# Kernel tuning notes

Measured on AMD Instinct MI355X. Metric: run time of the kernel, lower is better.

## Reference

```python
import jax, jax.numpy as jnp
import numpy as np

E = 2048      # embedding_size
H = 16        # num_heads
D = 128       # head_dim
G = 4         # gqa_factor
KH = H // G   # kv heads
F = 8192      # up_proj_size
B, S = 2, 2048


def _layer_norm(x, g, b, eps=1e-5):
    mu = jnp.mean(x, axis=-1, keepdims=True)
    var = jnp.mean(jnp.square(x - mu), axis=-1, keepdims=True)
    return (x - mu) * jax.lax.rsqrt(var + eps) * g + b


def setup_inputs() -> dict:
    key = jax.random.key(0)
    ks = jax.random.split(key, 16)
    std = 0.02
    inp = {
        'x': jax.random.normal(ks[0], (B, S, E), dtype=jnp.float32),
        'ln1_g': jnp.ones((E,), jnp.float32),
        'ln1_b': jnp.zeros((E,), jnp.float32),
        'wq': jax.random.normal(ks[1], (E, H * D), jnp.float32) * std,
        'bq': jnp.zeros((H * D,), jnp.float32),
        'wk': jax.random.normal(ks[2], (E, KH * D), jnp.float32) * std,
        'bk': jnp.zeros((KH * D,), jnp.float32),
        'wv': jax.random.normal(ks[3], (E, KH * D), jnp.float32) * std,
        'bv': jnp.zeros((KH * D,), jnp.float32),
        'wo': jax.random.normal(ks[4], (H * D, E), jnp.float32) * std,
        'bo': jnp.zeros((E,), jnp.float32),
        'ln2_g': jnp.ones((E,), jnp.float32),
        'ln2_b': jnp.zeros((E,), jnp.float32),
        'wu': jax.random.normal(ks[5], (E, F), jnp.float32) * std,
        'bu': jnp.zeros((F,), jnp.float32),
        'wd': jax.random.normal(ks[6], (F, E), jnp.float32) * std,
        'bd': jnp.zeros((E,), jnp.float32),
    }
    return inp


def _block(x, ln1_g, ln1_b, wq, bq, wk, bk, wv, bv, wo, bo, ln2_g, ln2_b, wu, bu, wd, bd):
    b, s, e = x.shape
    # attention sub-block (use_cache=False, train_mode=False -> no dropout)
    x1 = _layer_norm(x, ln1_g, ln1_b)
    q = (x1 @ wq + bq).reshape(b, s, H, D).transpose(0, 2, 1, 3)       # (B,H,S,D)
    q = q.reshape(b, KH, G, s, D)                                       # (B,KH,G,S,D)
    k = (x1 @ wk + bk).reshape(b, s, KH, D).transpose(0, 2, 1, 3)      # (B,KH,S,D)
    v = (x1 @ wv + bv).reshape(b, s, KH, D).transpose(0, 2, 1, 3)      # (B,KH,S,D)
    scores = jnp.einsum('bkgsd,bktd->bkgst', q, k) / np.sqrt(D).astype(np.float32)
    causal = jnp.tril(jnp.ones((s, s), dtype=bool))                     # True = keep
    scores = jnp.where(causal, scores, -jnp.inf)
    att = jax.nn.softmax(scores, axis=-1)
    o = jnp.einsum('bkgst,bktd->bkgsd', att, v)                         # (B,KH,G,S,D)
    o = o.reshape(b, H, s, D).transpose(0, 2, 1, 3).reshape(b, s, H * D)
    x = x + (o @ wo + bo)
    # MLP sub-block
    x2 = _layer_norm(x, ln2_g, ln2_b)
    h = jax.nn.gelu(x2 @ wu + bu, approximate=False)
    x = x + (h @ wd + bd)
    return x


def reference(x, ln1_g, ln1_b, wq, bq, wk, bk, wv, bv, wo, bo, ln2_g, ln2_b, wu, bu, wd, bd):
    return _block(x, ln1_g, ln1_b, wq, bq, wk, bk, wv, bv, wo, bo, ln2_g, ln2_b, wu, bu, wd, bd)
```

## Files before the change

kernel.cpp:

```cpp
#include <hip/hip_runtime.h>
#include <hip/hip_bf16.h>
#include <cstdint>
#include <math.h>

typedef unsigned short u16;
using f32x4   = __attribute__((ext_vector_type(4))) float;
using short8  = __attribute__((ext_vector_type(8))) short;
using short4v = __attribute__((ext_vector_type(4))) short;

#define DEV static __device__ __forceinline__

DEV u16 f2bf(float f) {
  union { float f; unsigned u; } v; v.f = f;
  unsigned r = v.u + 0x7fffu + ((v.u >> 16) & 1u);
  return (u16)(r >> 16);
}

DEV f32x4 mfma_bf16(short8 a, short8 b, f32x4 c) {
  return __builtin_amdgcn_mfma_f32_16x16x32_bf16(a, b, c, 0, 0, 0);
}

DEV void gload16(const void* g, void* l) {
  __builtin_amdgcn_global_load_lds((const __attribute__((address_space(1))) void*)g,
                                   (__attribute__((address_space(3))) void*)l,
                                   16, 0, 0);
}

__global__ __launch_bounds__(256) void prep_kernel(
    const float* __restrict__ x, const float* __restrict__ g,
    const float* __restrict__ bt, u16* __restrict__ x1,
    const float* __restrict__ wq, const float* __restrict__ wk,
    const float* __restrict__ wv, const float* __restrict__ wo,
    const float* __restrict__ wu, const float* __restrict__ wd,
    u16* __restrict__ wqT, u16* __restrict__ wkT, u16* __restrict__ wvT,
    u16* __restrict__ woT, u16* __restrict__ wuT, u16* __restrict__ wdT)
{
  __shared__ float sm[32 * 33];
  int bid = blockIdx.x;
  const int t = threadIdx.x;

  if (bid < 4096) {
    const int lane = t & 63, w = t >> 6;
    const float* xr = x + (size_t)bid * 2048 + t * 8;
    float v[8];
    {
      const float4* p4 = (const float4*)xr;
      float4 a = p4[0], b = p4[1];
      v[0] = a.x; v[1] = a.y; v[2] = a.z; v[3] = a.w;
      v[4] = b.x; v[5] = b.y; v[6] = b.z; v[7] = b.w;
    }
    float s = 0.f;
#pragma unroll
    for (int j = 0; j < 8; j++) s += v[j];
#pragma unroll
    for (int m = 1; m < 64; m <<= 1) s += __shfl_xor(s, m);
    if (lane == 0) sm[w] = s;
    __syncthreads();
    const float mu = (sm[0] + sm[1] + sm[2] + sm[3]) * (1.f / 2048.f);
    float q = 0.f;
#pragma unroll
    for (int j = 0; j < 8; j++) { v[j] -= mu; q += v[j] * v[j]; }
#pragma unroll
    for (int m = 1; m < 64; m <<= 1) q += __shfl_xor(q, m);
    if (lane == 0) sm[4 + w] = q;
    __syncthreads();
    const float rstd = rsqrtf((sm[4] + sm[5] + sm[6] + sm[7]) * (1.f / 2048.f) + 1e-5f);
    const float4* g4 = (const float4*)(g + t * 8);
    const float4* b4 = (const float4*)(bt + t * 8);
    float4 ga = g4[0], gb = g4[1], ba = b4[0], bb = b4[1];
    float gg[8] = {ga.x, ga.y, ga.z, ga.w, gb.x, gb.y, gb.z, gb.w};
    float bbv[8] = {ba.x, ba.y, ba.z, ba.w, bb.x, bb.y, bb.z, bb.w};
    short8 o;
#pragma unroll
    for (int j = 0; j < 8; j++) o[j] = (short)f2bf(v[j] * rstd * gg[j] + bbv[j]);
    *(short8*)&x1[(size_t)bid * 2048 + t * 8] = o;
    return;
  }
  bid -= 4096;

  const float* in; u16* outp; int K, N, bx, by;
  if (bid < 4096)              { in = wq; outp = wqT; K = 2048; N = 2048; bx = bid & 63;  by = bid >> 6; }
  else if ((bid -= 4096) < 1024)  { in = wk; outp = wkT; K = 2048; N = 512;  bx = bid & 15;  by = bid >> 4; }
  else if ((bid -= 1024) < 1024)  { in = wv; outp = wvT; K = 2048; N = 512;  bx = bid & 15;  by = bid >> 4; }
  else if ((bid -= 1024) < 4096)  { in = wo; outp = woT; K = 2048; N = 2048; bx = bid & 63;  by = bid >> 6; }
  else if ((bid -= 4096) < 16384) { in = wu; outp = wuT; K = 2048; N = 8192; bx = bid & 255; by = bid >> 8; }
  else { bid -= 16384;            in = wd; outp = wdT; K = 8192; N = 2048; bx = bid & 63;  by = bid >> 6; }

  const int n0 = bx * 32, k0 = by * 32;
  {
    const int c = t & 31, r = t >> 5;
#pragma unroll
    for (int i = 0; i < 4; i++)
      sm[(r + i * 8) * 33 + c] = in[(size_t)(k0 + r + i * 8) * N + n0 + c];
  }
  __syncthreads();
  {
    const int c4 = (t & 7) * 4, r = t >> 3;
    short4v o;
#pragma unroll
    for (int j = 0; j < 4; j++) o[j] = (short)f2bf(sm[(c4 + j) * 33 + r]);
    *(short4v*)&outp[(size_t)(n0 + r) * K + k0 + c4] = o;
  }
}

__global__ __launch_bounds__(256) void ln_kernel(
    const float* __restrict__ x, const float* __restrict__ g,
    const float* __restrict__ bt, u16* __restrict__ out)
{
  __shared__ float red1[4], red2[4];
  const int row = blockIdx.x;
  const int t = threadIdx.x;
  const int lane = t & 63, w = t >> 6;
  const float* xr = x + (size_t)row * 2048 + t * 8;
  float v[8];
  {
    const float4* p4 = (const float4*)xr;
    float4 a = p4[0], b = p4[1];
    v[0] = a.x; v[1] = a.y; v[2] = a.z; v[3] = a.w;
    v[4] = b.x; v[5] = b.y; v[6] = b.z; v[7] = b.w;
  }
  float s = 0.f;
#pragma unroll
  for (int j = 0; j < 8; j++) s += v[j];
#pragma unroll
  for (int m = 1; m < 64; m <<= 1) s += __shfl_xor(s, m);
  if (lane == 0) red1[w] = s;
  __syncthreads();
  const float mu = (red1[0] + red1[1] + red1[2] + red1[3]) * (1.f / 2048.f);
  float q = 0.f;
#pragma unroll
  for (int j = 0; j < 8; j++) { v[j] -= mu; q += v[j] * v[j]; }
#pragma unroll
  for (int m = 1; m < 64; m <<= 1) q += __shfl_xor(q, m);
  if (lane == 0) red2[w] = q;
  __syncthreads();
  const float rstd = rsqrtf((red2[0] + red2[1] + red2[2] + red2[3]) * (1.f / 2048.f) + 1e-5f);
  const float4* g4 = (const float4*)(g + t * 8);
  const float4* b4 = (const float4*)(bt + t * 8);
  float4 ga = g4[0], gb = g4[1], ba = b4[0], bb = b4[1];
  float gg[8] = {ga.x, ga.y, ga.z, ga.w, gb.x, gb.y, gb.z, gb.w};
  float bbv[8] = {ba.x, ba.y, ba.z, ba.w, bb.x, bb.y, bb.z, bb.w};
  short8 o;
#pragma unroll
  for (int j = 0; j < 8; j++) o[j] = (short)f2bf(v[j] * rstd * gg[j] + bbv[j]);
  *(short8*)&out[(size_t)row * 2048 + t * 8] = o;
}

template<int MODE, int N, int K, int STRIPE_N>
__global__ void __launch_bounds__(256) gemm_sb(
    const u16* __restrict__ A, const u16* __restrict__ Bt,
    const float* __restrict__ b0, const float* __restrict__ b1,
    const float* __restrict__ b2, const float* __restrict__ resid,
    u16* __restrict__ o0, u16* __restrict__ o1, u16* __restrict__ o2,
    float* __restrict__ of)
{
  __shared__ u16 As[128 * 64];
  __shared__ u16 Bs[128 * 64];
  constexpr int TN = N / 128;

  const int bid = blockIdx.x;
  const int xcd = bid & 7, wl = bid >> 3;
  int m0, n0;
  if constexpr (STRIPE_N) {
    constexpr int NSTR = TN / 8;
    n0 = (xcd * NSTR + (wl % NSTR)) * 128;
    m0 = (wl / NSTR) * 128;
  } else {
    m0 = (xcd * 4 + (wl & 3)) * 128;
    n0 = (wl >> 2) * 128;
  }
  const int tid = threadIdx.x;
  const int lane = tid & 63, w = tid >> 6;
  const int wm = w >> 1, wn = w & 1;
  const int z = lane >> 4, l15 = lane & 15;

  f32x4 acc[4][4];
#pragma unroll
  for (int m = 0; m < 4; m++)
#pragma unroll
    for (int n = 0; n < 4; n++)
#pragma unroll
      for (int i = 0; i < 4; i++) acc[m][n][i] = 0.f;

  for (int k0 = 0; k0 < K; k0 += 64) {
#pragma unroll
    for (int j = 0; j < 4; j++) {
      const int seg = w * 4 + j;
      const int c = seg * 64 + lane;
      const int r = c >> 3;
      const int cc = (c & 7) ^ (r & 7);
      gload16(A + (size_t)(m0 + r) * K + k0 + cc * 8, &As[seg * 512]);
    }
#pragma unroll
    for (int j = 0; j < 4; j++) {
      const int seg = w * 4 + j;
      const int c = seg * 64 + lane;
      const int r = c >> 3;
      const int cc = (c & 7) ^ (r & 7);
      gload16(Bt + (size_t)(n0 + r) * K + k0 + cc * 8, &Bs[seg * 512]);
    }
    asm volatile("s_waitcnt vmcnt(0)" ::: "memory");
    __syncthreads();

#pragma unroll
    for (int kk = 0; kk < 2; kk++) {
      short8 af[4], bfr[4];
#pragma unroll
      for (int m = 0; m < 4; m++) {
        const int row = wm * 64 + m * 16 + l15;
        const int off = row * 64 + ((kk * 32 + z * 8) ^ ((row & 7) << 3));
        af[m] = *(const short8*)&As[off];
      }
#pragma unroll
      for (int n = 0; n < 4; n++) {
        const int row = wn * 64 + n * 16 + l15;
        const int off = row * 64 + ((kk * 32 + z * 8) ^ ((row & 7) << 3));
        bfr[n] = *(const short8*)&Bs[off];
      }
      __builtin_amdgcn_s_setprio(1);
#pragma unroll
      for (int m = 0; m < 4; m++)
#pragma unroll
        for (int n = 0; n < 4; n++)
          acc[m][n] = mfma_bf16(af[m], bfr[n], acc[m][n]);
      __builtin_amdgcn_s_setprio(0);
    }
    __syncthreads();
  }

#pragma unroll
  for (int m = 0; m < 4; m++) {
    const int row0 = m0 + wm * 64 + m * 16 + z * 4;
#pragma unroll
    for (int n = 0; n < 4; n++) {
      const int col = n0 + wn * 64 + n * 16 + l15;
      f32x4 v = acc[m][n];
      if constexpr (MODE == 6) {
        if (col < 2048) {
          const float bb = b0[col];
#pragma unroll
          for (int i = 0; i < 4; i++)
            o0[(size_t)(row0 + i) * 2048 + col] = f2bf((v[i] + bb) * 0.08838834764831845f);
        } else if (col < 2560) {
          const int ck = col - 2048;
          const float bb = b1[ck];
#pragma unroll
          for (int i = 0; i < 4; i++)
            o1[(size_t)(row0 + i) * 512 + ck] = f2bf(v[i] + bb);
        } else {
          const int cc = col - 2560;
          const float bb = b2[cc];
          const int kh = cc >> 7, d = cc & 127;
          const int bidx = row0 >> 11, sidx = row0 & 2047;
          u16* vrow = &o2[((size_t)(bidx * 4 + kh) * 128 + d) * 2048 + sidx];
          short4v pq;
#pragma unroll
          for (int i = 0; i < 4; i++) pq[i] = (short)f2bf(v[i] + bb);
          *(short4v*)vrow = pq;
        }
      } else {
        const float bb = b0[col];
#pragma unroll
        for (int i = 0; i < 4; i++) {
          const size_t idx = (size_t)(row0 + i) * N + col;
          of[idx] = v[i] + bb + resid[idx];
        }
      }
    }
  }
}

template<int MODE, int N, int K, int STRIPE_N>
__global__ void __launch_bounds__(256) gemm_p3(
    const u16* __restrict__ A, const u16* __restrict__ Bt,
    const float* __restrict__ b0,
    u16* __restrict__ o0, float* __restrict__ of)
{
  __shared__ u16 As[3][128 * 32];
  __shared__ u16 Bs[3][128 * 32];
  constexpr int TN = N / 128;
  constexpr int NT = K / 32;

  const int bid = blockIdx.x;
  const int xcd = bid & 7, wl = bid >> 3;
  int m0, n0;
  if constexpr (STRIPE_N) {
    constexpr int NSTR = TN / 8;
    n0 = (xcd * NSTR + (wl % NSTR)) * 128;
    m0 = (wl / NSTR) * 128;
  } else {
    m0 = (xcd * 4 + (wl & 3)) * 128;
    n0 = (wl >> 2) * 128;
  }
  const int tid = threadIdx.x;
  const int lane = tid & 63, w = tid >> 6;
  const int wm = w >> 1, wn = w & 1;
  const int z = lane >> 4, l15 = lane & 15;

  f32x4 acc[4][4];
#pragma unroll
  for (int m = 0; m < 4; m++)
#pragma unroll
    for (int n = 0; n < 4; n++)
#pragma unroll
      for (int i = 0; i < 4; i++) acc[m][n][i] = 0.f;

  auto stage = [&](int g) {
    const int sl = g % 3;
    const int kc = g * 32;
#pragma unroll
    for (int s = 0; s < 2; s++) {
      const int c = s * 256 + tid;
      const int r = c >> 2, q = c & 3;
      const int cg = q ^ ((r >> 1) & 3);
      gload16(A + (size_t)(m0 + r) * K + kc + cg * 8, &As[sl][c * 8]);
    }
#pragma unroll
    for (int s = 0; s < 2; s++) {
      const int c = s * 256 + tid;
      const int r = c >> 2, q = c & 3;
      const int cg = q ^ ((r >> 1) & 3);
      gload16(Bt + (size_t)(n0 + r) * K + kc + cg * 8, &Bs[sl][c * 8]);
    }
  };

  stage(0); stage(1);
  asm volatile("s_waitcnt vmcnt(4)" ::: "memory");
  __syncthreads();

  for (int t = 0; t < NT; t++) {
    const int sl = t % 3;
    if (t + 2 < NT) stage(t + 2);

    short8 af[4], bfr[4];
#pragma unroll
    for (int m = 0; m < 4; m++) {
      const int row = wm * 64 + m * 16 + l15;
      af[m] = *(const short8*)&As[sl][row * 32 + ((z ^ ((row >> 1) & 3)) * 8)];
    }
#pragma unroll
    for (int n = 0; n < 4; n++) {
      const int row = wn * 64 + n * 16 + l15;
      bfr[n] = *(const short8*)&Bs[sl][row * 32 + ((z ^ ((row >> 1) & 3)) * 8)];
    }
    __builtin_amdgcn_s_setprio(1);
#pragma unroll
    for (int m = 0; m < 4; m++)
#pragma unroll
      for (int n = 0; n < 4; n++)
        acc[m][n] = mfma_bf16(af[m], bfr[n], acc[m][n]);
    __builtin_amdgcn_s_setprio(0);

    if (t + 2 < NT) {
      asm volatile("s_waitcnt vmcnt(4)" ::: "memory");
      __syncthreads();
    } else if (t + 1 < NT) {
      asm volatile("s_waitcnt vmcnt(0)" ::: "memory");
      __syncthreads();
    }
  }

#pragma unroll
  for (int m = 0; m < 4; m++) {
    const int row0 = m0 + wm * 64 + m * 16 + z * 4;
#pragma unroll
    for (int n = 0; n < 4; n++) {
      const int col = n0 + wn * 64 + n * 16 + l15;
      f32x4 v = acc[m][n];
      const float bb = b0[col];
      if constexpr (MODE == 4) {
#pragma unroll
        for (int i = 0; i < 4; i++) {
          const float xx = v[i] + bb;
          o0[(size_t)(row0 + i) * N + col] =
              f2bf(0.5f * xx * (1.f + erff(xx * 0.70710678118654752f)));
        }
      } else {
#pragma unroll
        for (int i = 0; i < 4; i++) {
          const size_t idx = (size_t)(row0 + i) * N + col;
          of[idx] = v[i] + bb + of[idx];
        }
      }
    }
  }
}

__global__ void __launch_bounds__(256) attn_kernel(
    const u16* __restrict__ qb, const u16* __restrict__ kb,
    const u16* __restrict__ vt, u16* __restrict__ ob)
{
  __shared__ u16 Kt[2][64 * 128];
  __shared__ u16 Vs[2][128 * 64];
  __shared__ u16 Pl[4 * 32 * 64];

  const int idx = blockIdx.x;
  const int xcd = idx & 7;
  const int u = (idx >> 3) & 31;
  const int half = idx >> 8;
  const int bh = xcd * 4 + (u & 3);
  const int qh = u >> 2;
  const int qt = half ? (15 - qh) : qh;

  const int b = bh >> 4, h = bh & 15, kh = h >> 2;
  const int q0 = qt * 128;
  const int tid = threadIdx.x, lane = tid & 63, w = tid >> 6;
  const int z = lane >> 4, l15 = lane & 15;
  const int qw0 = q0 + w * 32;
  const int ksw = (l15 & 7) << 3;

  short8 qf[2][4];
#pragma unroll
  for (int m = 0; m < 2; m++)
#pragma unroll
    for (int kk = 0; kk < 4; kk++)
      qf[m][kk] = *(const short8*)&qb[(size_t)(b * 2048 + qw0 + m * 16 + l15) * 2048 +
                                      h * 128 + kk * 32 + z * 8];

  f32x4 oacc[2][8];
#pragma unroll
  for (int m = 0; m < 2; m++)
#pragma unroll
    for (int n = 0; n < 8; n++)
#pragma unroll
      for (int i = 0; i < 4; i++) oacc[m][n][i] = 0.f;
  float mst[2][4], lst[2][4];
#pragma unroll
  for (int m = 0; m < 2; m++)
#pragma unroll
    for (int i = 0; i < 4; i++) { mst[m][i] = -1e30f; lst[m][i] = 0.f; }

  auto STAGE = [&](int tt, int bufsel) {
    const int kv0s = tt * 64;
#pragma unroll
    for (int j = 0; j < 4; j++) {
      const int seg = w * 4 + j;
      const int c = seg * 64 + lane;
      const int r = c >> 4;
      const int cc = (c & 15) ^ (r & 7);
      gload16(kb + (size_t)(b * 2048 + kv0s + r) * 512 + kh * 128 + cc * 8,
              &Kt[bufsel][seg * 512]);
    }
#pragma unroll
    for (int j = 0; j < 4; j++) {
      const int seg = w * 4 + j;
      const int c = seg * 64 + lane;
      const int d = c >> 3;
      const int cc = (c & 7) ^ (d & 7);
      gload16(vt + (size_t)((b * 4 + kh) * 128 + d) * 2048 + kv0s + cc * 8,
              &Vs[bufsel][seg * 512]);
    }
  };

  const int ntiles = q0 / 64 + 2;

  STAGE(0, 0);
  asm volatile("s_waitcnt vmcnt(0)" ::: "memory");
  __syncthreads();

  for (int t = 0; t < ntiles; t++) {
    const int cur = t & 1;
    if (t + 1 < ntiles) STAGE(t + 1, cur ^ 1);

    const int kv0 = t * 64;
    if (kv0 <= qw0 + 31) {
      f32x4 sf[2][4];
#pragma unroll
      for (int m = 0; m < 2; m++)
#pragma unroll
        for (int n = 0; n < 4; n++)
#pragma unroll
          for (int i = 0; i < 4; i++) sf[m][n][i] = 0.f;

      __builtin_amdgcn_s_setprio(1);
#pragma unroll
      for (int kk = 0; kk < 4; kk++) {
        short8 kfr[4];
#pragma unroll
        for (int n = 0; n < 4; n++) {
          const int row = n * 16 + l15;
          kfr[n] = *(const short8*)&Kt[cur][row * 128 + ((kk * 32 + z * 8) ^ ksw)];
        }
#pragma unroll
        for (int m = 0; m < 2; m++)
#pragma unroll
          for (int n = 0; n < 4; n++)
            sf[m][n] = mfma_bf16(qf[m][kk], kfr[n], sf[m][n]);
      }
      __builtin_amdgcn_s_setprio(0);

      u16* Pw = &Pl[w * 2048];
      const bool edge = (kv0 + 63 > qw0);
#pragma unroll
      for (int m = 0; m < 2; m++) {
#pragma unroll
        for (int i = 0; i < 4; i++) {
          const int rq = qw0 + m * 16 + z * 4 + i;
          if (edge) {
#pragma unroll
            for (int n = 0; n < 4; n++)
              if (kv0 + n * 16 + l15 > rq) sf[m][n][i] = -1e30f;
          }
          float mx = fmaxf(fmaxf(sf[m][0][i], sf[m][1][i]), fmaxf(sf[m][2][i], sf[m][3][i]));
          mx = fmaxf(mx, __shfl_xor(mx, 1));
          mx = fmaxf(mx, __shfl_xor(mx, 2));
          mx = fmaxf(mx, __shfl_xor(mx, 4));
          mx = fmaxf(mx, __shfl_xor(mx, 8));
          const bool grow = mx > mst[m][i];
          const float mn = grow ? mx : mst[m][i];
          float rs = 0.f;
#pragma unroll
          for (int n = 0; n < 4; n++) {
            const float p = __expf(sf[m][n][i] - mn);
            sf[m][n][i] = p;
            rs += p;
          }
          rs += __shfl_xor(rs, 1);
          rs += __shfl_xor(rs, 2);
          rs += __shfl_xor(rs, 4);
          rs += __shfl_xor(rs, 8);
          if (grow) {
            const float al = __expf(mst[m][i] - mx);
            mst[m][i] = mx;
            lst[m][i] = lst[m][i] * al + rs;
#pragma unroll
            for (int n = 0; n < 8; n++) oacc[m][n][i] *= al;
          } else {
            lst[m][i] += rs;
          }
          const int prow = m * 16 + z * 4 + i;
          const int psw = ((z * 4 + i) & 7) << 3;
#pragma unroll
          for (int n = 0; n < 4; n++)
            Pw[prow * 64 + ((n * 16 + l15) ^ psw)] = f2bf(sf[m][n][i]);
        }
      }

      __builtin_amdgcn_s_setprio(1);
#pragma unroll
      for (int kk = 0; kk < 2; kk++) {
        short8 af[2], vf[8];
#pragma unroll
        for (int m = 0; m < 2; m++) {
          const int row = m * 16 + l15;
          af[m] = *(const short8*)&Pw[row * 64 + ((kk * 32 + z * 8) ^ ksw)];
        }
#pragma unroll
        for (int n = 0; n < 8; n++) {
          const int row = n * 16 + l15;
          vf[n] = *(const short8*)&Vs[cur][row * 64 + ((kk * 32 + z * 8) ^ ksw)];
        }
#pragma unroll
        for (int m = 0; m < 2; m++)
#pragma unroll
          for (int n = 0; n < 8; n++)
            oacc[m][n] = mfma_bf16(af[m], vf[n], oacc[m][n]);
      }
      __builtin_amdgcn_s_setprio(0);
    }

    asm volatile("s_waitcnt vmcnt(0)" ::: "memory");
    __syncthreads();
  }

#pragma unroll
  for (int m = 0; m < 2; m++)
#pragma unroll
    for (int i = 0; i < 4; i++) {
      const float inv = 1.0f / lst[m][i];
      const int rq = qw0 + m * 16 + z * 4 + i;
      u16* orow = &ob[(size_t)(b * 2048 + rq) * 2048 + h * 128];
#pragma unroll
      for (int n = 0; n < 8; n++)
        orow[n * 16 + l15] = f2bf(oacc[m][n][i] * inv);
    }
}

extern "C" void kernel_launch(void* const* d_in, const int* in_sizes, int n_in,
                              void* d_out, int out_size, void* d_ws, size_t ws_size,
                              hipStream_t stream) {
  (void)in_sizes; (void)n_in; (void)out_size; (void)ws_size;
  const float* x     = (const float*)d_in[0];
  const float* ln1_g = (const float*)d_in[1];
  const float* ln1_b = (const float*)d_in[2];
  const float* wq    = (const float*)d_in[3];
  const float* bq    = (const float*)d_in[4];
  const float* wk    = (const float*)d_in[5];
  const float* bk    = (const float*)d_in[6];
  const float* wv    = (const float*)d_in[7];
  const float* bv    = (const float*)d_in[8];
  const float* wo    = (const float*)d_in[9];
  const float* bo    = (const float*)d_in[10];
  const float* ln2_g = (const float*)d_in[11];
  const float* ln2_b = (const float*)d_in[12];
  const float* wu    = (const float*)d_in[13];
  const float* bu    = (const float*)d_in[14];
  const float* wd    = (const float*)d_in[15];
  const float* bd    = (const float*)d_in[16];
  float* out = (float*)d_out;

  char* p = (char*)d_ws;
  u16* wqT = (u16*)p; p += (size_t)2048 * 2048 * 2;
  u16* wkT = (u16*)p; p += (size_t)512 * 2048 * 2;
  u16* wvT = (u16*)p; p += (size_t)512 * 2048 * 2;
  u16* woT = (u16*)p; p += (size_t)2048 * 2048 * 2;
  u16* wuT = (u16*)p; p += (size_t)8192 * 2048 * 2;
  u16* wdT = (u16*)p; p += (size_t)2048 * 8192 * 2;
  u16* x1  = (u16*)p; p += (size_t)4096 * 2048 * 2;
  u16* qbuf= (u16*)p; p += (size_t)4096 * 2048 * 2;
  u16* kbuf= (u16*)p; p += (size_t)4096 * 512 * 2;
  u16* vtb = (u16*)p; p += (size_t)4096 * 512 * 2;
  u16* hb  = (u16*)p; p += (size_t)4096 * 8192 * 2;
  u16* ob  = x1;
  u16* x2  = qbuf;

  prep_kernel<<<47104, 256, 0, stream>>>(
      x, ln1_g, ln1_b, x1, wq, wk, wv, wo, wu, wd,
      wqT, wkT, wvT, woT, wuT, wdT);

  gemm_sb<6, 3072, 2048, 0><<<768, 256, 0, stream>>>(
      x1, wqT, bq, bk, bv, nullptr, qbuf, kbuf, vtb, nullptr);

  attn_kernel<<<512, 256, 0, stream>>>(qbuf, kbuf, vtb, ob);

  gemm_sb<3, 2048, 2048, 0><<<512, 256, 0, stream>>>(
      ob, woT, bo, nullptr, nullptr, x, nullptr, nullptr, nullptr, out);

  ln_kernel<<<4096, 256, 0, stream>>>(out, ln2_g, ln2_b, x2);

  gemm_p3<4, 8192, 2048, 1><<<2048, 256, 0, stream>>>(x2, wuT, bu, hb, nullptr);
  gemm_p3<5, 2048, 8192, 1><<<512, 256, 0, stream>>>(hb, wdT, bd, nullptr, out);
}
```

Before: 776.0 us.

## Switch MLP GEMMs to double-buffered 64-wide K tiles with 8-way XOR swizzle

```diff
diff --git a/kernel.cpp b/kernel.cpp
--- a/kernel.cpp
+++ b/kernel.cpp
@@ -271,15 +271,15 @@
 }
 
 template<int MODE, int N, int K, int STRIPE_N>
-__global__ void __launch_bounds__(256) gemm_p3(
+__global__ void __launch_bounds__(256) gemm_db(
     const u16* __restrict__ A, const u16* __restrict__ Bt,
     const float* __restrict__ b0,
     u16* __restrict__ o0, float* __restrict__ of)
 {
-  __shared__ u16 As[3][128 * 32];
-  __shared__ u16 Bs[3][128 * 32];
+  __shared__ u16 As[2][128 * 64];
+  __shared__ u16 Bs[2][128 * 64];
   constexpr int TN = N / 128;
-  constexpr int NT = K / 32;
+  constexpr int NT = K / 64;
 
   const int bid = blockIdx.x;
   const int xcd = bid & 7, wl = bid >> 3;
@@ -305,59 +305,60 @@
 #pragma unroll
       for (int i = 0; i < 4; i++) acc[m][n][i] = 0.f;
 
-  auto stage = [&](int g) {
-    const int sl = g % 3;
-    const int kc = g * 32;
-#pragma unroll
-    for (int s = 0; s < 2; s++) {
-      const int c = s * 256 + tid;
-      const int r = c >> 2, q = c & 3;
-      const int cg = q ^ ((r >> 1) & 3);
-      gload16(A + (size_t)(m0 + r) * K + kc + cg * 8, &As[sl][c * 8]);
-    }
-#pragma unroll
-    for (int s = 0; s < 2; s++) {
-      const int c = s * 256 + tid;
-      const int r = c >> 2, q = c & 3;
-      const int cg = q ^ ((r >> 1) & 3);
-      gload16(Bt + (size_t)(n0 + r) * K + kc + cg * 8, &Bs[sl][c * 8]);
+  auto stage = [&](int k0, int buf) {
+#pragma unroll
+    for (int j = 0; j < 4; j++) {
+      const int seg = w * 4 + j;
+      const int c = seg * 64 + lane;
+      const int r = c >> 3;
+      const int cc = (c & 7) ^ (r & 7);
+      gload16(A + (size_t)(m0 + r) * K + k0 + cc * 8, &As[buf][seg * 512]);
+    }
+#pragma unroll
+    for (int j = 0; j < 4; j++) {
+      const int seg = w * 4 + j;
+      const int c = seg * 64 + lane;
+      const int r = c >> 3;
+      const int cc = (c & 7) ^ (r & 7);
+      gload16(Bt + (size_t)(n0 + r) * K + k0 + cc * 8, &Bs[buf][seg * 512]);
     }
   };
 
-  stage(0); stage(1);
-  asm volatile("s_waitcnt vmcnt(4)" ::: "memory");
+  stage(0, 0);
+  asm volatile("s_waitcnt vmcnt(0)" ::: "memory");
   __syncthreads();
 
+  int cur = 0;
   for (int t = 0; t < NT; t++) {
-    const int sl = t % 3;
-    if (t + 2 < NT) stage(t + 2);
-
-    short8 af[4], bfr[4];
-#pragma unroll
-    for (int m = 0; m < 4; m++) {
-      const int row = wm * 64 + m * 16 + l15;
-      af[m] = *(const short8*)&As[sl][row * 32 + ((z ^ ((row >> 1) & 3)) * 8)];
-    }
-#pragma unroll
-    for (int n = 0; n < 4; n++) {
-      const int row = wn * 64 + n * 16 + l15;
-      bfr[n] = *(const short8*)&Bs[sl][row * 32 + ((z ^ ((row >> 1) & 3)) * 8)];
-    }
-    __builtin_amdgcn_s_setprio(1);
-#pragma unroll
-    for (int m = 0; m < 4; m++)
-#pragma unroll
-      for (int n = 0; n < 4; n++)
-        acc[m][n] = mfma_bf16(af[m], bfr[n], acc[m][n]);
-    __builtin_amdgcn_s_setprio(0);
-
-    if (t + 2 < NT) {
-      asm volatile("s_waitcnt vmcnt(4)" ::: "memory");
-      __syncthreads();
-    } else if (t + 1 < NT) {
-      asm volatile("s_waitcnt vmcnt(0)" ::: "memory");
-      __syncthreads();
-    }
+    if (t + 1 < NT) stage((t + 1) * 64, cur ^ 1);
+
+#pragma unroll
+    for (int kk = 0; kk < 2; kk++) {
+      short8 af[4], bfr[4];
+#pragma unroll
+      for (int m = 0; m < 4; m++) {
+        const int row = wm * 64 + m * 16 + l15;
+        const int off = row * 64 + ((kk * 32 + z * 8) ^ ((row & 7) << 3));
+        af[m] = *(const short8*)&As[cur][off];
+      }
+#pragma unroll
+      for (int n = 0; n < 4; n++) {
+        const int row = wn * 64 + n * 16 + l15;
+        const int off = row * 64 + ((kk * 32 + z * 8) ^ ((row & 7) << 3));
+        bfr[n] = *(const short8*)&Bs[cur][off];
+      }
+      __builtin_amdgcn_s_setprio(1);
+#pragma unroll
+      for (int m = 0; m < 4; m++)
+#pragma unroll
+        for (int n = 0; n < 4; n++)
+          acc[m][n] = mfma_bf16(af[m], bfr[n], acc[m][n]);
+      __builtin_amdgcn_s_setprio(0);
+    }
+
+    asm volatile("s_waitcnt vmcnt(0)" ::: "memory");
+    __syncthreads();
+    cur ^= 1;
   }
 
 #pragma unroll
@@ -628,6 +629,6 @@
 
   ln_kernel<<<4096, 256, 0, stream>>>(out, ln2_g, ln2_b, x2);
 
-  gemm_p3<4, 8192, 2048, 1><<<2048, 256, 0, stream>>>(x2, wuT, bu, hb, nullptr);
-  gemm_p3<5, 2048, 8192, 1><<<512, 256, 0, stream>>>(hb, wdT, bd, nullptr, out);
-}
+  gemm_db<4, 8192, 2048, 1><<<2048, 256, 0, stream>>>(x2, wuT, bu, hb, nullptr);
+  gemm_db<5, 2048, 8192, 1><<<512, 256, 0, stream>>>(hb, wdT, bd, nullptr, out);
+}
```

New measurement: 712.6 us. -8.2%, faster.
